# Performance work log

Measured on AMD Instinct MI355X. Metric: run time of the kernel, lower is better.

## Reference

```python
import jax, jax.numpy as jnp
import numpy as np

# NF4 codebook (bitsandbytes NormalFloat4 quantiles)
NF4_TABLE = jnp.array([
    -1.0, -0.6961928009986877, -0.5250730514526367, -0.39491748809814453,
    -0.28444138169288635, -0.18477343022823334, -0.09105003625154495, 0.0,
    0.07958029955625534, 0.16093020141124725, 0.24611230194568634,
    0.33791524171829224, 0.44070982933044434, 0.5626170039176941,
    0.7229568362236023, 1.0], dtype=jnp.float32)

BLOCK = 64  # bitsandbytes default quantization blocksize


def setup_inputs() -> dict:
    key = jax.random.key(0)
    ks = jax.random.split(key, 6)
    in_f, out_f, rank, n_tok = 4096, 4096, 16, 8192
    x = jax.random.normal(ks[0], (n_tok, in_f), dtype=jnp.float32)
    q_codes = jax.random.randint(ks[1], (out_f, in_f), 0, 16, dtype=jnp.int32)
    absmax = jax.random.uniform(ks[2], (out_f, in_f // BLOCK), dtype=jnp.float32) * 0.1 + 1e-3
    bias = jax.random.normal(ks[3], (out_f,), dtype=jnp.float32) * 0.02
    # kaiming-uniform-ish init for lora_down; lora_up nonzero for a meaningful test
    lora_down_w = jax.random.normal(ks[4], (rank, in_f), dtype=jnp.float32) * (1.0 / np.sqrt(in_f))
    lora_up_w = jax.random.normal(ks[5], (out_f, rank), dtype=jnp.float32) * 0.02
    alpha = jnp.array(16.0, dtype=jnp.float32)
    return {"x": x, "absmax": absmax, "bias": bias, "lora_down_w": lora_down_w,
            "lora_up_w": lora_up_w, "alpha": alpha, "q_codes": q_codes}


def reference(x, absmax, bias, lora_down_w, lora_up_w, alpha, q_codes):
    rank = lora_down_w.shape[0]
    # dequantize NF4 base weight: code lookup * per-block absmax scale
    w = NF4_TABLE[q_codes] * jnp.repeat(absmax, BLOCK, axis=1)  # [out, in]
    base = x @ w.T + bias                                       # [n_tok, out]
    # LoRA path: down [rank,in], up [out,rank], scaled by alpha/rank
    lora = (x @ lora_down_w.T) @ lora_up_w.T                    # [n_tok, out]
    return base + lora * (alpha / rank)
```

## Files before the change

kernel.cpp:

```cpp
#include <hip/hip_runtime.h>

#define IN_F 4096
#define OUT_F 4096
#define RANK 16
#define NTOK 8192
#define KP 4160
#define BK 64
#define NT (KP / BK)
#define BM 256
#define BN 256

typedef __bf16 bf16x8 __attribute__((ext_vector_type(8)));
typedef float f32x4 __attribute__((ext_vector_type(4)));

__device__ __forceinline__ unsigned short f2bf(float f) {
  unsigned int u = __float_as_uint(f);
  u += 0x7fffu + ((u >> 16) & 1u);
  return (unsigned short)(u >> 16);
}

__device__ __forceinline__ void async_ld16(const void* g, void* l) {
  __builtin_amdgcn_global_load_lds(
      (const __attribute__((address_space(1))) unsigned int*)g,
      (__attribute__((address_space(3))) unsigned int*)l, 16, 0, 0);
}

__device__ const float NF4_TAB[16] = {
    -1.0f, -0.6961928009986877f, -0.5250730514526367f, -0.39491748809814453f,
    -0.28444138169288635f, -0.18477343022823334f, -0.09105003625154495f, 0.0f,
    0.07958029955625534f, 0.16093020141124725f, 0.24611230194568634f,
    0.33791524171829224f, 0.44070982933044434f, 0.5626170039176941f,
    0.7229568362236023f, 1.0f};

__global__ __launch_bounds__(256) void k_prep_a(
    const float* __restrict__ x, const float* __restrict__ ldw,
    unsigned short* __restrict__ Ap) {
  const int tid = threadIdx.x;
  const int lane = tid & 63;
  const int w = tid >> 6;
  const int m0 = blockIdx.x * 4;

  float acc[4][4];
#pragma unroll
  for (int i = 0; i < 4; ++i)
#pragma unroll
    for (int rl = 0; rl < 4; ++rl) acc[i][rl] = 0.f;

  for (int c = 0; c < 16; ++c) {
    const int k0 = (c * 64 + lane) * 4;
    float4 xv[4];
#pragma unroll
    for (int i = 0; i < 4; ++i) {
      xv[i] = *(const float4*)&x[(size_t)(m0 + i) * IN_F + k0];
      if (w == i) {
        ushort4 s;
        s.x = f2bf(xv[i].x); s.y = f2bf(xv[i].y);
        s.z = f2bf(xv[i].z); s.w = f2bf(xv[i].w);
        *(ushort4*)&Ap[(size_t)(m0 + i) * KP + k0] = s;
      }
    }
#pragma unroll
    for (int rl = 0; rl < 4; ++rl) {
      float4 lv = *(const float4*)&ldw[(size_t)(w * 4 + rl) * IN_F + k0];
#pragma unroll
      for (int i = 0; i < 4; ++i)
        acc[i][rl] += xv[i].x * lv.x + xv[i].y * lv.y + xv[i].z * lv.z +
                      xv[i].w * lv.w;
    }
  }
#pragma unroll
  for (int i = 0; i < 4; ++i)
#pragma unroll
    for (int rl = 0; rl < 4; ++rl) {
      float v = acc[i][rl];
#pragma unroll
      for (int m = 1; m < 64; m <<= 1) v += __shfl_xor(v, m, 64);
      acc[i][rl] = v;
    }
  __shared__ float red[4][16];
  if (lane == 0) {
#pragma unroll
    for (int i = 0; i < 4; ++i)
#pragma unroll
      for (int rl = 0; rl < 4; ++rl) red[i][w * 4 + rl] = acc[i][rl];
  }
  __syncthreads();
  if (tid < 64) {
    Ap[(size_t)(m0 + (tid >> 4)) * KP + IN_F + (tid & 15)] =
        f2bf(red[tid >> 4][tid & 15]);
  } else {
    const int t2 = tid - 64;
    if (t2 < 192)
      Ap[(size_t)(m0 + t2 / 48) * KP + IN_F + 16 + (t2 % 48)] = 0;
  }
}

__global__ __launch_bounds__(256) void k_prep_b(
    const int* __restrict__ q, const float* __restrict__ amax,
    const float* __restrict__ luw, const float* __restrict__ alpha,
    unsigned short* __restrict__ Bp) {
  __shared__ float tab[16];
  const int tid = threadIdx.x;
  const int n = blockIdx.x;
  if (tid < 16) tab[tid] = NF4_TAB[tid];
  __syncthreads();
#pragma unroll
  for (int c = 0; c < 4; ++c) {
    const int k0 = (tid + 256 * c) * 4;
    int4 qv = *(const int4*)&q[(size_t)n * IN_F + k0];
    float am = amax[n * (IN_F / 64) + (k0 >> 6)];
    ushort4 s;
    s.x = f2bf(tab[qv.x] * am);
    s.y = f2bf(tab[qv.y] * am);
    s.z = f2bf(tab[qv.z] * am);
    s.w = f2bf(tab[qv.w] * am);
    *(ushort4*)&Bp[(size_t)n * KP + k0] = s;
  }
  if (tid < RANK) {
    float sc = alpha[0] * (1.0f / RANK);
    Bp[(size_t)n * KP + IN_F + tid] = f2bf(luw[n * RANK + tid] * sc);
  } else if (tid < 64) {
    Bp[(size_t)n * KP + IN_F + tid] = 0;
  }
}

__global__ __launch_bounds__(512, 1) void k_gemm(
    const unsigned short* __restrict__ Ap, const unsigned short* __restrict__ Bp,
    const float* __restrict__ bias, float* __restrict__ out) {
  __shared__ unsigned short lds[65536];
  const int tid = threadIdx.x;
  const int lane = tid & 63;
  const int w = tid >> 6;
  const int wr = w >> 2;
  const int wc = w & 3;

  const int flat = blockIdx.x;
  const int swz = (flat & 7) * 64 + (flat >> 3);
  const int m0 = (swz >> 4) * BM;
  const int n0 = (swz & 15) * BN;

  const int srow = lane >> 3;
  const int scol = (((lane & 7) ^ srow) << 3);
  const unsigned short* gA = Ap + (size_t)(m0 + (w << 4) + srow) * KP + scol;
  const unsigned short* gB = Bp + (size_t)(n0 + (w << 4) + srow) * KP + scol;
  unsigned short* const ldsw = lds + (w << 10);

  const int rdoff = ((lane & 15) << 6) + (((lane >> 4) ^ (lane & 7)) << 3);

#define STAGE2(tt, ht, cond)                                                   \
  if (cond) {                                                                  \
    const unsigned short* s_ =                                                 \
        ((ht) < 2 ? gA + (size_t)((ht) << 7) * KP                              \
                  : gB + (size_t)(((ht)-2) << 7) * KP) + (size_t)(tt)*BK;      \
    unsigned short* d_ = ldsw + ((((tt)&1) << 15) + ((ht) << 13));             \
    async_ld16(s_, d_);                                                        \
    async_ld16(s_ + (size_t)8 * KP, d_ + 512);                                 \
  }

#define LDA(bsel, mh, f, kc)                                                   \
  (*(const bf16x8*)&lds[((bsel) << 15) + (wr << 13) +                          \
                        (((mh)*64 + (f)*16) << 6) + (((kc) << 5) ^ rdoff)])
#define LDB(bsel, nh, g, kc)                                                   \
  (*(const bf16x8*)&lds[((bsel) << 15) + ((2 + (wc >> 1)) << 13) +             \
                        ((((wc & 1) * 64) + (nh)*32 + (g)*16) << 6) +          \
                        (((kc) << 5) ^ rdoff)])

#define MFMA(a, b, c) __builtin_amdgcn_mfma_f32_16x16x32_bf16((a), (b), (c), 0, 0, 0)
#define SG(mask, n) __builtin_amdgcn_sched_group_barrier((mask), (n), 0)

  STAGE2(0, 2, true) STAGE2(0, 3, true) STAGE2(0, 0, true) STAGE2(0, 1, true)
  STAGE2(1, 2, true) STAGE2(1, 3, true) STAGE2(1, 0, true) STAGE2(1, 1, true)
  asm volatile("s_waitcnt vmcnt(8)" ::: "memory");
  __builtin_amdgcn_s_barrier();

  f32x4 acc[8][4] = {};
  bf16x8 a0[4][2], a1[4][2], b0[2][2], b1[2][2];

#pragma unroll
  for (int g = 0; g < 2; ++g) {
    b0[g][0] = LDB(0, 0, g, 0);
    b0[g][1] = LDB(0, 0, g, 1);
  }
#pragma unroll
  for (int f = 0; f < 4; ++f) {
    a0[f][0] = LDA(0, 0, f, 0);
    a0[f][1] = LDA(0, 0, f, 1);
  }

#pragma unroll 2
  for (int t = 0; t < NT; ++t) {
    const int bsel = t & 1;
#pragma unroll
    for (int g = 0; g < 2; ++g) {
      b1[g][0] = LDB(bsel, 1, g, 0);
      b1[g][1] = LDB(bsel, 1, g, 1);
    }
#pragma unroll
    for (int f = 0; f < 2; ++f) {
      a1[f][0] = LDA(bsel, 1, f, 0);
      a1[f][1] = LDA(bsel, 1, f, 1);
    }
#pragma unroll
    for (int f = 0; f < 4; ++f)
#pragma unroll
      for (int g = 0; g < 2; ++g) {
        acc[f][g] = MFMA(a0[f][0], b0[g][0], acc[f][g]);
        acc[f][g] = MFMA(a0[f][1], b0[g][1], acc[f][g]);
      }
#pragma unroll
    for (int i = 0; i < 8; ++i) { SG(0x100, 1); SG(0x8, 2); }
#pragma unroll
    for (int f = 2; f < 4; ++f) {
      a1[f][0] = LDA(bsel, 1, f, 0);
      a1[f][1] = LDA(bsel, 1, f, 1);
    }
#pragma unroll
    for (int f = 0; f < 4; ++f)
#pragma unroll
      for (int g = 0; g < 2; ++g) {
        acc[f][2 + g] = MFMA(a0[f][0], b1[g][0], acc[f][2 + g]);
        acc[f][2 + g] = MFMA(a0[f][1], b1[g][1], acc[f][2 + g]);
      }
#pragma unroll
    for (int i = 0; i < 4; ++i) { SG(0x100, 1); SG(0x8, 4); }
    __builtin_amdgcn_s_barrier();
    STAGE2(t + 2, 2, t + 2 < NT)
    STAGE2(t + 2, 3, t + 2 < NT)
#pragma unroll
    for (int f = 0; f < 4; ++f)
#pragma unroll
      for (int g = 0; g < 2; ++g) {
        acc[4 + f][2 + g] = MFMA(a1[f][0], b1[g][0], acc[4 + f][2 + g]);
        acc[4 + f][2 + g] = MFMA(a1[f][1], b1[g][1], acc[4 + f][2 + g]);
      }
    SG(0x10, 4); SG(0x8, 16);
    if (t < NT - 2) {
      asm volatile("s_waitcnt vmcnt(4)" ::: "memory");
    } else {
      asm volatile("s_waitcnt vmcnt(0)" ::: "memory");
    }
    __builtin_amdgcn_s_barrier();
    STAGE2(t + 2, 0, t + 2 < NT)
    STAGE2(t + 2, 1, t + 2 < NT)
    if (t + 1 < NT) {
#pragma unroll
      for (int f = 0; f < 4; ++f) {
        a0[f][0] = LDA(bsel ^ 1, 0, f, 0);
        a0[f][1] = LDA(bsel ^ 1, 0, f, 1);
      }
    }
#pragma unroll
    for (int f = 0; f < 4; ++f)
#pragma unroll
      for (int g = 0; g < 2; ++g) {
        acc[4 + f][g] = MFMA(a1[f][0], b0[g][0], acc[4 + f][g]);
        acc[4 + f][g] = MFMA(a1[f][1], b0[g][1], acc[4 + f][g]);
      }
    if (t + 1 < NT) {
#pragma unroll
      for (int g = 0; g < 2; ++g) {
        b0[g][0] = LDB(bsel ^ 1, 0, g, 0);
        b0[g][1] = LDB(bsel ^ 1, 0, g, 1);
      }
    }
    SG(0x10, 4);
#pragma unroll
    for (int i = 0; i < 8; ++i) { SG(0x100, 1); SG(0x8, 2); }
    SG(0x100, 4);
  }

  const int colL = lane & 15;
  const int rowG = lane >> 4;
#pragma unroll
  for (int nj = 0; nj < 4; ++nj) {
    const int n = n0 + wc * 64 + nj * 16 + colL;
    const float bv = bias[n];
#pragma unroll
    for (int mi = 0; mi < 8; ++mi) {
      const int mb = m0 + wr * 128 + mi * 16 + rowG * 4;
#pragma unroll
      for (int e = 0; e < 4; ++e)
        out[(size_t)(mb + e) * OUT_F + n] = acc[mi][nj][e] + bv;
    }
  }
#undef STAGE2
#undef LDA
#undef LDB
#undef MFMA
#undef SG
}

extern "C" void kernel_launch(void* const* d_in, const int* in_sizes, int n_in,
                              void* d_out, int out_size, void* d_ws, size_t ws_size,
                              hipStream_t stream) {
  (void)in_sizes; (void)n_in; (void)out_size; (void)ws_size;
  const float* x     = (const float*)d_in[0];
  const float* amax  = (const float*)d_in[1];
  const float* bias  = (const float*)d_in[2];
  const float* ldw   = (const float*)d_in[3];
  const float* luw   = (const float*)d_in[4];
  const float* alpha = (const float*)d_in[5];
  const int*   q     = (const int*)d_in[6];
  float* out = (float*)d_out;

  unsigned short* Ap = (unsigned short*)d_ws;
  unsigned short* Bp = Ap + (size_t)NTOK * KP;

  k_prep_a<<<NTOK / 4, 256, 0, stream>>>(x, ldw, Ap);
  k_prep_b<<<OUT_F, 256, 0, stream>>>(q, amax, luw, alpha, Bp);
  k_gemm<<<512, 512, 0, stream>>>(Ap, Bp, bias, out);
}
```

Before: 326.8 us.

## Restructure GEMM main loop with double-buffered B fragments and MFMA priority

Rewrites the K-loop body as a macro that is manually unrolled by two. It ping-pongs two B-fragment register sets so the next tile's B and A fragments are loaded from LDS before the final MFMA quadrant rather than after it. It also splits the a1 × b1 quadrant around the second barrier, moves a0[2..3] loads to the tile start, and wraps MFMA groups in s_setprio to raise wave priority. The aim is better overlap of LDS reads with MFMA work across waves, at the cost of more VGPRs and a more fragile schedule.

After: 410.1 us. +25.5%, slower.

```diff
diff --git a/kernel.cpp b/kernel.cpp
--- a/kernel.cpp
+++ b/kernel.cpp
@@ -167,106 +167,106 @@
 
 #define MFMA(a, b, c) __builtin_amdgcn_mfma_f32_16x16x32_bf16((a), (b), (c), 0, 0, 0)
 #define SG(mask, n) __builtin_amdgcn_sched_group_barrier((mask), (n), 0)
+#define BAR() __builtin_amdgcn_s_barrier()
 
   STAGE2(0, 2, true) STAGE2(0, 3, true) STAGE2(0, 0, true) STAGE2(0, 1, true)
   STAGE2(1, 2, true) STAGE2(1, 3, true) STAGE2(1, 0, true) STAGE2(1, 1, true)
   asm volatile("s_waitcnt vmcnt(8)" ::: "memory");
-  __builtin_amdgcn_s_barrier();
+  BAR();
 
   f32x4 acc[8][4] = {};
-  bf16x8 a0[4][2], a1[4][2], b0[2][2], b1[2][2];
+  bf16x8 a0[4][2], a1[4][2], b1[2][2], b0A[2][2], b0B[2][2];
 
 #pragma unroll
   for (int g = 0; g < 2; ++g) {
-    b0[g][0] = LDB(0, 0, g, 0);
-    b0[g][1] = LDB(0, 0, g, 1);
-  }
-#pragma unroll
-  for (int f = 0; f < 4; ++f) {
+    b0A[g][0] = LDB(0, 0, g, 0);
+    b0A[g][1] = LDB(0, 0, g, 1);
+  }
+#pragma unroll
+  for (int f = 0; f < 2; ++f) {
     a0[f][0] = LDA(0, 0, f, 0);
     a0[f][1] = LDA(0, 0, f, 1);
   }
 
-#pragma unroll 2
-  for (int t = 0; t < NT; ++t) {
-    const int bsel = t & 1;
-#pragma unroll
-    for (int g = 0; g < 2; ++g) {
-      b1[g][0] = LDB(bsel, 1, g, 0);
-      b1[g][1] = LDB(bsel, 1, g, 1);
-    }
-#pragma unroll
-    for (int f = 0; f < 2; ++f) {
-      a1[f][0] = LDA(bsel, 1, f, 0);
-      a1[f][1] = LDA(bsel, 1, f, 1);
-    }
-#pragma unroll
-    for (int f = 0; f < 4; ++f)
-#pragma unroll
-      for (int g = 0; g < 2; ++g) {
-        acc[f][g] = MFMA(a0[f][0], b0[g][0], acc[f][g]);
-        acc[f][g] = MFMA(a0[f][1], b0[g][1], acc[f][g]);
-      }
-#pragma unroll
-    for (int i = 0; i < 8; ++i) { SG(0x100, 1); SG(0x8, 2); }
-#pragma unroll
-    for (int f = 2; f < 4; ++f) {
-      a1[f][0] = LDA(bsel, 1, f, 0);
-      a1[f][1] = LDA(bsel, 1, f, 1);
-    }
-#pragma unroll
-    for (int f = 0; f < 4; ++f)
-#pragma unroll
-      for (int g = 0; g < 2; ++g) {
-        acc[f][2 + g] = MFMA(a0[f][0], b1[g][0], acc[f][2 + g]);
-        acc[f][2 + g] = MFMA(a0[f][1], b1[g][1], acc[f][2 + g]);
-      }
-#pragma unroll
-    for (int i = 0; i < 4; ++i) { SG(0x100, 1); SG(0x8, 4); }
-    __builtin_amdgcn_s_barrier();
-    STAGE2(t + 2, 2, t + 2 < NT)
-    STAGE2(t + 2, 3, t + 2 < NT)
-#pragma unroll
-    for (int f = 0; f < 4; ++f)
-#pragma unroll
-      for (int g = 0; g < 2; ++g) {
-        acc[4 + f][2 + g] = MFMA(a1[f][0], b1[g][0], acc[4 + f][2 + g]);
-        acc[4 + f][2 + g] = MFMA(a1[f][1], b1[g][1], acc[4 + f][2 + g]);
-      }
-    SG(0x10, 4); SG(0x8, 16);
-    if (t < NT - 2) {
-      asm volatile("s_waitcnt vmcnt(4)" ::: "memory");
-    } else {
-      asm volatile("s_waitcnt vmcnt(0)" ::: "memory");
-    }
-    __builtin_amdgcn_s_barrier();
-    STAGE2(t + 2, 0, t + 2 < NT)
-    STAGE2(t + 2, 1, t + 2 < NT)
+#define TILEBODY(T, BC, BN_)                                                   \
+  {                                                                            \
+    const int bsel = (T) & 1;                                                  \
+            \
+    a0[2][0] = LDA(bsel, 0, 2, 0); a0[2][1] = LDA(bsel, 0, 2, 1);              \
+    a0[3][0] = LDA(bsel, 0, 3, 0); a0[3][1] = LDA(bsel, 0, 3, 1);              \
+    b1[0][0] = LDB(bsel, 1, 0, 0); b1[0][1] = LDB(bsel, 1, 0, 1);              \
+    b1[1][0] = LDB(bsel, 1, 1, 0); b1[1][1] = LDB(bsel, 1, 1, 1);              \
+    __builtin_amdgcn_s_setprio(1);                                             \
+    _Pragma("unroll") for (int f = 0; f < 4; ++f)                              \
+        _Pragma("unroll") for (int g = 0; g < 2; ++g) {                        \
+      acc[f][g] = MFMA(a0[f][0], BC[g][0], acc[f][g]);                         \
+      acc[f][g] = MFMA(a0[f][1], BC[g][1], acc[f][g]);                         \
+    }                                                                          \
+    __builtin_amdgcn_s_setprio(0);                                             \
+    _Pragma("unroll") for (int i = 0; i < 8; ++i) { SG(0x100, 1); SG(0x8, 2); }\
+                                     \
+    _Pragma("unroll") for (int f = 0; f < 4; ++f) {                            \
+      a1[f][0] = LDA(bsel, 1, f, 0); a1[f][1] = LDA(bsel, 1, f, 1);            \
+    }                                                                          \
+    __builtin_amdgcn_s_setprio(1);                                             \
+    _Pragma("unroll") for (int f = 0; f < 4; ++f)                              \
+        _Pragma("unroll") for (int g = 0; g < 2; ++g) {                        \
+      acc[f][2 + g] = MFMA(a0[f][0], b1[g][0], acc[f][2 + g]);                 \
+      acc[f][2 + g] = MFMA(a0[f][1], b1[g][1], acc[f][2 + g]);                 \
+    }                                                                          \
+    __builtin_amdgcn_s_setprio(0);                                             \
+    _Pragma("unroll") for (int i = 0; i < 8; ++i) { SG(0x100, 1); SG(0x8, 2); }\
+    BAR();                                    \
+                             \
+    STAGE2((T) + 2, 2, (T) + 2 < NT)                                           \
+    STAGE2((T) + 2, 3, (T) + 2 < NT)                                           \
+    __builtin_amdgcn_s_setprio(1);                                             \
+    _Pragma("unroll") for (int f = 0; f < 2; ++f)                              \
+        _Pragma("unroll") for (int g = 0; g < 2; ++g) {                        \
+      acc[4 + f][2 + g] = MFMA(a1[f][0], b1[g][0], acc[4 + f][2 + g]);         \
+      acc[4 + f][2 + g] = MFMA(a1[f][1], b1[g][1], acc[4 + f][2 + g]);         \
+    }                                                                          \
+    __builtin_amdgcn_s_setprio(0);                                             \
+    SG(0x10, 4); SG(0x8, 8);                                                   \
+    if ((T) + 2 < NT) {                                                        \
+      asm volatile("s_waitcnt vmcnt(4)" ::: "memory");                         \
+    } else {                                                                   \
+      asm volatile("s_waitcnt vmcnt(0)" ::: "memory");                         \
+    }                                                                          \
+    BAR();                         \
+              \
+    if ((T) + 1 < NT) {                                                        \
+      BN_[0][0] = LDB(bsel ^ 1, 0, 0, 0); BN_[0][1] = LDB(bsel ^ 1, 0, 0, 1);  \
+      BN_[1][0] = LDB(bsel ^ 1, 0, 1, 0); BN_[1][1] = LDB(bsel ^ 1, 0, 1, 1);  \
+      a0[0][0] = LDA(bsel ^ 1, 0, 0, 0); a0[0][1] = LDA(bsel ^ 1, 0, 0, 1);    \
+      a0[1][0] = LDA(bsel ^ 1, 0, 1, 0); a0[1][1] = LDA(bsel ^ 1, 0, 1, 1);    \
+    }                                                                          \
+    __builtin_amdgcn_s_setprio(1);                                             \
+    _Pragma("unroll") for (int f = 2; f < 4; ++f)                              \
+        _Pragma("unroll") for (int g = 0; g < 2; ++g) {                        \
+      acc[4 + f][2 + g] = MFMA(a1[f][0], b1[g][0], acc[4 + f][2 + g]);         \
+      acc[4 + f][2 + g] = MFMA(a1[f][1], b1[g][1], acc[4 + f][2 + g]);         \
+    }                                                                          \
+    __builtin_amdgcn_s_setprio(0);                                             \
+    _Pragma("unroll") for (int i = 0; i < 8; ++i) { SG(0x100, 1); SG(0x8, 1); }\
+                   \
+    STAGE2((T) + 2, 0, (T) + 2 < NT)                                           \
+    STAGE2((T) + 2, 1, (T) + 2 < NT)                                           \
+    __builtin_amdgcn_s_setprio(1);                                             \
+    _Pragma("unroll") for (int f = 0; f < 4; ++f)                              \
+        _Pragma("unroll") for (int g = 0; g < 2; ++g) {                        \
+      acc[4 + f][g] = MFMA(a1[f][0], BC[g][0], acc[4 + f][g]);                 \
+      acc[4 + f][g] = MFMA(a1[f][1], BC[g][1], acc[4 + f][g]);                 \
+    }                                                                          \
+    __builtin_amdgcn_s_setprio(0);                                             \
+    SG(0x10, 4); SG(0x8, 16);                                                  \
+  }
+
+  for (int t = 0; t < NT; t += 2) {
+    TILEBODY(t, b0A, b0B)
     if (t + 1 < NT) {
-#pragma unroll
-      for (int f = 0; f < 4; ++f) {
-        a0[f][0] = LDA(bsel ^ 1, 0, f, 0);
-        a0[f][1] = LDA(bsel ^ 1, 0, f, 1);
-      }
-    }
-#pragma unroll
-    for (int f = 0; f < 4; ++f)
-#pragma unroll
-      for (int g = 0; g < 2; ++g) {
-        acc[4 + f][g] = MFMA(a1[f][0], b0[g][0], acc[4 + f][g]);
-        acc[4 + f][g] = MFMA(a1[f][1], b0[g][1], acc[4 + f][g]);
-      }
-    if (t + 1 < NT) {
-#pragma unroll
-      for (int g = 0; g < 2; ++g) {
-        b0[g][0] = LDB(bsel ^ 1, 0, g, 0);
-        b0[g][1] = LDB(bsel ^ 1, 0, g, 1);
-      }
-    }
-    SG(0x10, 4);
-#pragma unroll
-    for (int i = 0; i < 8; ++i) { SG(0x100, 1); SG(0x8, 2); }
-    SG(0x100, 4);
+      TILEBODY(t + 1, b0B, b0A)
+    }
   }
 
   const int colL = lane & 15;
@@ -283,11 +283,13 @@
         out[(size_t)(mb + e) * OUT_F + n] = acc[mi][nj][e] + bv;
     }
   }
+#undef TILEBODY
 #undef STAGE2
 #undef LDA
 #undef LDB
 #undef MFMA
 #undef SG
+#undef BAR
 }
 
 extern "C" void kernel_launch(void* const* d_in, const int* in_sizes, int n_in,
```

## Give each wave its own four rows in k_prep_a and drop LDS reduction

Applied to the files above, without the earlier changes.

Each wavefront in k_prep_a now owns four token rows and computes all 16 LoRA-down dot products for them, instead of four waves sharing four rows and splitting the rank. This removes the redundant x loads across waves, the shared-memory reduction and __syncthreads, and quarters the grid size. In exchange each thread holds 64 accumulators and does more shuffle reductions, which raises register pressure and may lower occupancy; ldw is reread per wave but stays in cache.

Measured after the change: 359.7 us. 1.1x slower.

```diff
diff --git a/kernel.cpp b/kernel.cpp
--- a/kernel.cpp
+++ b/kernel.cpp
@@ -38,13 +38,13 @@
   const int tid = threadIdx.x;
   const int lane = tid & 63;
   const int w = tid >> 6;
-  const int m0 = blockIdx.x * 4;
-
-  float acc[4][4];
+  const int m0 = blockIdx.x * 16 + w * 4;
+
+  float dot[4][16];
 #pragma unroll
   for (int i = 0; i < 4; ++i)
 #pragma unroll
-    for (int rl = 0; rl < 4; ++rl) acc[i][rl] = 0.f;
+    for (int r = 0; r < 16; ++r) dot[i][r] = 0.f;
 
   for (int c = 0; c < 16; ++c) {
     const int k0 = (c * 64 + lane) * 4;
@@ -52,46 +52,47 @@
 #pragma unroll
     for (int i = 0; i < 4; ++i) {
       xv[i] = *(const float4*)&x[(size_t)(m0 + i) * IN_F + k0];
-      if (w == i) {
-        ushort4 s;
-        s.x = f2bf(xv[i].x); s.y = f2bf(xv[i].y);
-        s.z = f2bf(xv[i].z); s.w = f2bf(xv[i].w);
-        *(ushort4*)&Ap[(size_t)(m0 + i) * KP + k0] = s;
-      }
-    }
-#pragma unroll
-    for (int rl = 0; rl < 4; ++rl) {
-      float4 lv = *(const float4*)&ldw[(size_t)(w * 4 + rl) * IN_F + k0];
+      ushort4 s;
+      s.x = f2bf(xv[i].x); s.y = f2bf(xv[i].y);
+      s.z = f2bf(xv[i].z); s.w = f2bf(xv[i].w);
+      *(ushort4*)&Ap[(size_t)(m0 + i) * KP + k0] = s;
+    }
+#pragma unroll
+    for (int r = 0; r < 16; ++r) {
+      float4 lv = *(const float4*)&ldw[(size_t)r * IN_F + k0];
 #pragma unroll
       for (int i = 0; i < 4; ++i)
-        acc[i][rl] += xv[i].x * lv.x + xv[i].y * lv.y + xv[i].z * lv.z +
-                      xv[i].w * lv.w;
+        dot[i][r] += xv[i].x * lv.x + xv[i].y * lv.y + xv[i].z * lv.z +
+                     xv[i].w * lv.w;
     }
   }
 #pragma unroll
   for (int i = 0; i < 4; ++i)
 #pragma unroll
-    for (int rl = 0; rl < 4; ++rl) {
-      float v = acc[i][rl];
-#pragma unroll
-      for (int m = 1; m < 64; m <<= 1) v += __shfl_xor(v, m, 64);
-      acc[i][rl] = v;
-    }
-  __shared__ float red[4][16];
-  if (lane == 0) {
-#pragma unroll
-    for (int i = 0; i < 4; ++i)
-#pragma unroll
-      for (int rl = 0; rl < 4; ++rl) red[i][w * 4 + rl] = acc[i][rl];
-  }
-  __syncthreads();
-  if (tid < 64) {
-    Ap[(size_t)(m0 + (tid >> 4)) * KP + IN_F + (tid & 15)] =
-        f2bf(red[tid >> 4][tid & 15]);
-  } else {
-    const int t2 = tid - 64;
-    if (t2 < 192)
-      Ap[(size_t)(m0 + t2 / 48) * KP + IN_F + 16 + (t2 % 48)] = 0;
+    for (int r = 0; r < 16; ++r) {
+      float v = dot[i][r];
+#pragma unroll
+      for (int mm = 1; mm < 64; mm <<= 1) v += __shfl_xor(v, mm, 64);
+      dot[i][r] = v;
+    }
+#pragma unroll
+  for (int i = 0; i < 4; ++i) {
+    unsigned short val = 0;
+    if (lane < 16) {
+      float dv;
+      switch (lane) {
+        case 0: dv = dot[i][0]; break;   case 1: dv = dot[i][1]; break;
+        case 2: dv = dot[i][2]; break;   case 3: dv = dot[i][3]; break;
+        case 4: dv = dot[i][4]; break;   case 5: dv = dot[i][5]; break;
+        case 6: dv = dot[i][6]; break;   case 7: dv = dot[i][7]; break;
+        case 8: dv = dot[i][8]; break;   case 9: dv = dot[i][9]; break;
+        case 10: dv = dot[i][10]; break; case 11: dv = dot[i][11]; break;
+        case 12: dv = dot[i][12]; break; case 13: dv = dot[i][13]; break;
+        case 14: dv = dot[i][14]; break; default: dv = dot[i][15]; break;
+      }
+      val = f2bf(dv);
+    }
+    Ap[(size_t)(m0 + i) * KP + IN_F + lane] = val;
   }
 }
 
@@ -306,7 +307,7 @@
   unsigned short* Ap = (unsigned short*)d_ws;
   unsigned short* Bp = Ap + (size_t)NTOK * KP;
 
-  k_prep_a<<<NTOK / 4, 256, 0, stream>>>(x, ldw, Ap);
+  k_prep_a<<<NTOK / 16, 256, 0, stream>>>(x, ldw, Ap);
   k_prep_b<<<OUT_F, 256, 0, stream>>>(q, amax, luw, alpha, Bp);
   k_gemm<<<512, 512, 0, stream>>>(Ap, Bp, bias, out);
 }
```
